# Kernel optimization log

Hardware: AMD Instinct MI355X
Metric: run time of the kernel (lower is better)

Reference implementation:

```python
import jax, jax.numpy as jnp
from jax import lax
import numpy as np

B, T, C = 8, 16384, 64
NUM_FILTERS, FILTER_SIZE = 64, 5
LEAKY_SLOPE = 0.3  # keras activation 'leaky_relu' default negative_slope


def setup_inputs() -> dict:
    key = jax.random.key(0)
    k1, k2, k3 = jax.random.split(key, 3)
    x = jax.random.normal(k1, (B, T, C), dtype=jnp.float32)
    interp_weights = jax.random.normal(k2, (C,), dtype=jnp.float32)
    # Conv1D kernel layout: [filter_size, in_channels, out_channels]
    conv_kernel = jax.random.normal(k3, (FILTER_SIZE, C, NUM_FILTERS), dtype=jnp.float32) * 0.05
    conv_bias = jnp.zeros((NUM_FILTERS,), dtype=jnp.float32)
    return {"x": x, "interp_weights": interp_weights,
            "conv_kernel": conv_kernel, "conv_bias": conv_bias}


def reference(x, interp_weights, conv_kernel, conv_bias):
    # Sigmoid gate per channel
    w = jax.nn.sigmoid(interp_weights)  # [C]
    # The diag conv2d (filter [1,2,C,C], SAME) is: blend[t] = w*x[t] + (1-w)*x[t+1]
    # (TF SAME for even width pads one zero frame on the right)
    x_next = jnp.concatenate([x[:, 1:, :], jnp.zeros_like(x[:, :1, :])], axis=1)
    blend = w * x + (1.0 - w) * x_next  # [B, T, C]
    # Interleave: even positions original, odd positions blended -> [B, 2T, C]
    up = jnp.stack([x, blend], axis=2).reshape(B, 2 * T, C)
    # Conv1D(num_filters, filter_size, padding='same', stride 1) + leaky_relu
    y = lax.conv_general_dilated(
        up, conv_kernel,
        window_strides=(1,), padding='SAME',
        dimension_numbers=('NWC', 'WIO', 'NWC'))
    y = y + conv_bias
    return jnp.where(y >= 0, y, LEAKY_SLOPE * y)
```

## Files before the change

### kernel.cpp

```cpp
#include <hip/hip_runtime.h>
#include <hip/hip_bf16.h>
#include <cstdint>


#define T_ 16384
#define TWO_T 32768
#define WSLICE 1376
#define XSTRIDE 72

typedef __bf16 bf16x8 __attribute__((ext_vector_type(8)));
typedef float  f32x4  __attribute__((ext_vector_type(4)));
typedef unsigned short u16x8 __attribute__((ext_vector_type(8)));
typedef unsigned short u16x4 __attribute__((ext_vector_type(4)));

__device__ __forceinline__ unsigned short f2bf(float f) {
    union { float f; uint32_t u; } v; v.f = f;
    uint32_t u = v.u;
    return (unsigned short)((u + 0x7FFFu + ((u >> 16) & 1u)) >> 16);
}

__device__ __forceinline__ float sigmoidf_(float z) {
    return 1.0f / (1.0f + expf(-z));
}

__global__ void lu_prep_kernel(const float* __restrict__ iw,
                               const float* __restrict__ ck,
                               const float* __restrict__ x,
                               unsigned short* __restrict__ bp,
                               float* __restrict__ corrf) {
    int fi = blockIdx.x;
    int l  = threadIdx.x;
    if (fi < 56) {
        int phase, ks, nt;
        if (fi < 24) { phase = 0; ks = fi >> 2; nt = fi & 3; }
        else         { phase = 1; ks = (fi - 24) >> 2; nt = (fi - 24) & 3; }
        int tap = ks >> 1;
        int n   = nt * 16 + (l & 15);
        int c0  = ((ks & 1) << 5) + ((l >> 4) << 3);
        u16x8 pk;
#pragma unroll
        for (int i = 0; i < 8; ++i) {
            int c = c0 + i;
            float w = sigmoidf_(iw[c]);
            float v;
            #define CK(k) ck[((k) * 64 + c) * 64 + n]
            if (phase == 0) {
                if (tap == 0)      v = CK(0) + w * CK(1);
                else if (tap == 1) v = (1.f - w) * CK(1) + CK(2) + w * CK(3);
                else               v = (1.f - w) * CK(3) + CK(4);
            } else {
                if (tap == 0)      v = w * CK(0);
                else if (tap == 1) v = (1.f - w) * CK(0) + CK(1) + w * CK(2);
                else if (tap == 2) v = (1.f - w) * CK(2) + CK(3) + w * CK(4);
                else               v = (1.f - w) * CK(4);
            }
            #undef CK
            pk[i] = f2bf(v);
        }
        *(u16x8*)(bp + (((size_t)fi * 64) + l) * 8) = pk;
    } else {
        int b = fi - 56;
        int f = l;
        float cE = 0.f, cO = 0.f;
        for (int c = 0; c < 64; ++c) {
            float w = sigmoidf_(iw[c]);
            float g = (1.f - w) * x[(size_t)b * T_ * 64 + c];
            cE += ck[(64 + c) * 64 + f] * g;
            cO += ck[c * 64 + f] * g;
        }
        corrf[b * 128 + f]      = cE;
        corrf[b * 128 + 64 + f] = cO;
    }
}

__global__ __launch_bounds__(256) void lu_main_kernel(
        const float* __restrict__ x,
        const unsigned short* __restrict__ bp,
        const float* __restrict__ corrf,
        const float* __restrict__ bias,
        float* __restrict__ out) {
    __shared__ __align__(16) unsigned short xl[4][WSLICE];

    const int wid  = blockIdx.x;
    const int b    = wid >> 10;
    const int win  = wid & 1023;
    const int tw0  = win << 4;
    const int tid  = threadIdx.x;
    const int lane = tid & 63;
    const int wv   = tid >> 6;

    unsigned short* xw = &xl[wv][0];

#pragma unroll
    for (int it = 0; it < 5; ++it) {
        int idx = it * 64 + lane;
        if (idx < 304) {
            int j  = idx >> 4;
            int c4 = (idx & 15) << 2;
            int gf = tw0 - 1 + j;
            float4 v = make_float4(0.f, 0.f, 0.f, 0.f);
            if (gf >= 0 && gf < T_)
                v = *(const float4*)(x + ((size_t)b * T_ + gf) * 64 + c4);
            u16x4 pk;
            pk[0] = f2bf(v.x); pk[1] = f2bf(v.y);
            pk[2] = f2bf(v.z); pk[3] = f2bf(v.w);
            *(u16x4*)(xw + j * XSTRIDE + c4) = pk;
        }
    }

    bf16x8 Be[6], Bo[8];
#pragma unroll
    for (int ks = 0; ks < 6; ++ks)
        Be[ks] = __builtin_bit_cast(bf16x8,
            *(const u16x8*)(bp + (((size_t)(ks * 4 + wv)) * 64 + lane) * 8));
#pragma unroll
    for (int ks = 0; ks < 8; ++ks)
        Bo[ks] = __builtin_bit_cast(bf16x8,
            *(const u16x8*)(bp + (((size_t)(24 + ks * 4 + wv)) * 64 + lane) * 8));

    const int   f      = (wv << 4) + (lane & 15);
    const float bias_f = bias[f];
    const int   arow   = lane & 15;
    const int   ac0    = (lane >> 4) << 3;

    bf16x8 Af[4][2];
#pragma unroll
    for (int tap = 0; tap < 4; ++tap)
#pragma unroll
        for (int h = 0; h < 2; ++h)
            Af[tap][h] = __builtin_bit_cast(bf16x8,
                *(const u16x8*)(xw + (arow + tap) * XSTRIDE + (h << 5) + ac0));

    f32x4 accE = {0.f, 0.f, 0.f, 0.f};
#pragma unroll
    for (int ks = 0; ks < 6; ++ks)
        accE = __builtin_amdgcn_mfma_f32_16x16x32_bf16(
                Af[ks >> 1][ks & 1], Be[ks], accE, 0, 0, 0);
    f32x4 accO = {0.f, 0.f, 0.f, 0.f};
#pragma unroll
    for (int ks = 0; ks < 8; ++ks)
        accO = __builtin_amdgcn_mfma_f32_16x16x32_bf16(
                Af[ks >> 1][ks & 1], Bo[ks], accO, 0, 0, 0);

    if (win == 0) {
        float cE = corrf[b * 128 + f];
        float cO = corrf[b * 128 + 64 + f];
        if ((lane >> 4) == 0) {
            accE[0] -= cE;
            accO[0] -= cO;
        }
    }

    const size_t ob = ((size_t)b * TWO_T + ((size_t)tw0 << 1)) * 64 + f;
#pragma unroll
    for (int i = 0; i < 4; ++i) {
        int r2 = (((lane >> 4) << 2) + i) << 1;
        float vE = accE[i] + bias_f;
        vE = vE >= 0.f ? vE : 0.3f * vE;
        out[ob + (size_t)r2 * 64] = vE;
        float vO = accO[i] + bias_f;
        vO = vO >= 0.f ? vO : 0.3f * vO;
        out[ob + (size_t)(r2 + 1) * 64] = vO;
    }
}

extern "C" void kernel_launch(void* const* d_in, const int* in_sizes, int n_in,
                              void* d_out, int out_size, void* d_ws, size_t ws_size,
                              hipStream_t stream) {
    (void)in_sizes; (void)n_in; (void)out_size; (void)ws_size;
    const float* x    = (const float*)d_in[0];
    const float* iw   = (const float*)d_in[1];
    const float* ck   = (const float*)d_in[2];
    const float* bias = (const float*)d_in[3];
    float* out = (float*)d_out;
    unsigned short* bp = (unsigned short*)d_ws;
    float* corrf = (float*)((char*)d_ws + 57344);

    lu_prep_kernel<<<64, 64, 0, stream>>>(iw, ck, x, bp, corrf);
    lu_main_kernel<<<8192, 256, 0, stream>>>(x, bp, corrf, bias, out);
}
```

Before: 39.84 us.

## Process four time windows per block with register-prefetched loads of the next window

Each block now handles 64 time steps as four 16-step windows instead of one, so the B-fragment weight loads are amortized over four windows. Global loads for the next window are issued into registers before the MFMAs of the current window run, to overlap memory latency with compute. The grid shrinks from 8192 to 2048 blocks, launch bounds add an occupancy hint, and the bf16 conversion uses the native cast. Risks include more register pressure and fewer blocks for latency hiding. There is also no barrier between a wave's LDS reads and its next overwrite of the same slice, which relies on in-order execution within a wave.

```diff
diff --git a/kernel.cpp b/kernel.cpp
--- a/kernel.cpp
+++ b/kernel.cpp
@@ -5,22 +5,22 @@
 
 #define T_ 16384
 #define TWO_T 32768
-#define WSLICE 1376
 #define XSTRIDE 72
+#define WSL 1376
 
 typedef __bf16 bf16x8 __attribute__((ext_vector_type(8)));
+typedef __bf16 bf16x4 __attribute__((ext_vector_type(4)));
 typedef float  f32x4  __attribute__((ext_vector_type(4)));
 typedef unsigned short u16x8 __attribute__((ext_vector_type(8)));
-typedef unsigned short u16x4 __attribute__((ext_vector_type(4)));
+
+__device__ __forceinline__ float sigmoidf_(float z) {
+    return 1.0f / (1.0f + expf(-z));
+}
 
 __device__ __forceinline__ unsigned short f2bf(float f) {
     union { float f; uint32_t u; } v; v.f = f;
     uint32_t u = v.u;
     return (unsigned short)((u + 0x7FFFu + ((u >> 16) & 1u)) >> 16);
-}
-
-__device__ __forceinline__ float sigmoidf_(float z) {
-    return 1.0f / (1.0f + expf(-z));
 }
 
 __global__ void lu_prep_kernel(const float* __restrict__ iw,
@@ -62,6 +62,7 @@
         int b = fi - 56;
         int f = l;
         float cE = 0.f, cO = 0.f;
+#pragma unroll
         for (int c = 0; c < 64; ++c) {
             float w = sigmoidf_(iw[c]);
             float g = (1.f - w) * x[(size_t)b * T_ * 64 + c];
@@ -73,40 +74,40 @@
     }
 }
 
-__global__ __launch_bounds__(256) void lu_main_kernel(
+__device__ __forceinline__ void issue_loads(const float* __restrict__ x,
+                                            int b, int t0, int lane, float4* ld) {
+#pragma unroll
+    for (int it = 0; it < 5; ++it) {
+        int idx = it * 64 + lane;
+        int j   = idx >> 4;
+        int c4  = (idx & 15) << 2;
+        int gf  = t0 - 1 + j;
+        float4 v = make_float4(0.f, 0.f, 0.f, 0.f);
+        if (idx < 304 && gf >= 0 && gf < T_)
+            v = *(const float4*)(x + ((size_t)b * T_ + gf) * 64 + c4);
+        ld[it] = v;
+    }
+}
+
+__global__ __launch_bounds__(256, 4) void lu_main_kernel(
         const float* __restrict__ x,
         const unsigned short* __restrict__ bp,
         const float* __restrict__ corrf,
         const float* __restrict__ bias,
         float* __restrict__ out) {
-    __shared__ __align__(16) unsigned short xl[4][WSLICE];
+    __shared__ __align__(16) unsigned short xl[4][WSL];
 
-    const int wid  = blockIdx.x;
-    const int b    = wid >> 10;
-    const int win  = wid & 1023;
-    const int tw0  = win << 4;
+    const int bid  = blockIdx.x;
+    const int b    = bid >> 8;
+    const int p0   = (bid & 255) << 6;
     const int tid  = threadIdx.x;
     const int lane = tid & 63;
     const int wv   = tid >> 6;
 
     unsigned short* xw = &xl[wv][0];
 
-#pragma unroll
-    for (int it = 0; it < 5; ++it) {
-        int idx = it * 64 + lane;
-        if (idx < 304) {
-            int j  = idx >> 4;
-            int c4 = (idx & 15) << 2;
-            int gf = tw0 - 1 + j;
-            float4 v = make_float4(0.f, 0.f, 0.f, 0.f);
-            if (gf >= 0 && gf < T_)
-                v = *(const float4*)(x + ((size_t)b * T_ + gf) * 64 + c4);
-            u16x4 pk;
-            pk[0] = f2bf(v.x); pk[1] = f2bf(v.y);
-            pk[2] = f2bf(v.z); pk[3] = f2bf(v.w);
-            *(u16x4*)(xw + j * XSTRIDE + c4) = pk;
-        }
-    }
+    float4 ld[5];
+    issue_loads(x, b, p0, lane, ld);
 
     bf16x8 Be[6], Bo[8];
 #pragma unroll
@@ -121,46 +122,57 @@
     const int   f      = (wv << 4) + (lane & 15);
     const float bias_f = bias[f];
     const int   arow   = lane & 15;
-    const int   ac0    = (lane >> 4) << 3;
+    const int   hi     = lane >> 4;
+    const int   ac0    = hi << 3;
 
-    bf16x8 Af[4][2];
+    for (int w = 0; w < 4; ++w) {
+        const int t0 = p0 + (w << 4);
+
 #pragma unroll
-    for (int tap = 0; tap < 4; ++tap)
+        for (int it = 0; it < 5; ++it) {
+            int idx = it * 64 + lane;
+            if (idx < 304) {
+                int j  = idx >> 4;
+                int c4 = (idx & 15) << 2;
+                bf16x4 pk;
+                pk[0] = (__bf16)ld[it].x; pk[1] = (__bf16)ld[it].y;
+                pk[2] = (__bf16)ld[it].z; pk[3] = (__bf16)ld[it].w;
+                *(bf16x4*)(xw + j * XSTRIDE + c4) = pk;
+            }
+        }
+
+        if (w < 3) issue_loads(x, b, p0 + ((w + 1) << 4), lane, ld);
+
+        f32x4 accE = {0.f, 0.f, 0.f, 0.f};
+        f32x4 accO = {0.f, 0.f, 0.f, 0.f};
 #pragma unroll
-        for (int h = 0; h < 2; ++h)
-            Af[tap][h] = __builtin_bit_cast(bf16x8,
-                *(const u16x8*)(xw + (arow + tap) * XSTRIDE + (h << 5) + ac0));
+        for (int tap = 0; tap < 4; ++tap)
+#pragma unroll
+            for (int h = 0; h < 2; ++h) {
+                bf16x8 a = __builtin_bit_cast(bf16x8,
+                    *(const u16x8*)(xw + (arow + tap) * XSTRIDE + (h << 5) + ac0));
+                int ks = tap * 2 + h;
+                if (tap < 3)
+                    accE = __builtin_amdgcn_mfma_f32_16x16x32_bf16(a, Be[ks], accE, 0, 0, 0);
+                accO = __builtin_amdgcn_mfma_f32_16x16x32_bf16(a, Bo[ks], accO, 0, 0, 0);
+            }
 
-    f32x4 accE = {0.f, 0.f, 0.f, 0.f};
+        if (((bid & 255) | w) == 0 && hi == 0) {
+            accE[0] -= corrf[b * 128 + f];
+            accO[0] -= corrf[b * 128 + 64 + f];
+        }
+
+        const size_t ob = ((size_t)b * TWO_T + ((size_t)t0 << 1)) * 64 + f;
 #pragma unroll
-    for (int ks = 0; ks < 6; ++ks)
-        accE = __builtin_amdgcn_mfma_f32_16x16x32_bf16(
-                Af[ks >> 1][ks & 1], Be[ks], accE, 0, 0, 0);
-    f32x4 accO = {0.f, 0.f, 0.f, 0.f};
-#pragma unroll
-    for (int ks = 0; ks < 8; ++ks)
-        accO = __builtin_amdgcn_mfma_f32_16x16x32_bf16(
-                Af[ks >> 1][ks & 1], Bo[ks], accO, 0, 0, 0);
-
-    if (win == 0) {
-        float cE = corrf[b * 128 + f];
-        float cO = corrf[b * 128 + 64 + f];
-        if ((lane >> 4) == 0) {
-            accE[0] -= cE;
-            accO[0] -= cO;
+        for (int i = 0; i < 4; ++i) {
+            int r2 = ((hi << 2) + i) << 1;
+            float vE = accE[i] + bias_f;
+            vE = vE >= 0.f ? vE : 0.3f * vE;
+            out[ob + (size_t)r2 * 64] = vE;
+            float vO = accO[i] + bias_f;
+            vO = vO >= 0.f ? vO : 0.3f * vO;
+            out[ob + (size_t)(r2 + 1) * 64] = vO;
         }
-    }
-
-    const size_t ob = ((size_t)b * TWO_T + ((size_t)tw0 << 1)) * 64 + f;
-#pragma unroll
-    for (int i = 0; i < 4; ++i) {
-        int r2 = (((lane >> 4) << 2) + i) << 1;
-        float vE = accE[i] + bias_f;
-        vE = vE >= 0.f ? vE : 0.3f * vE;
-        out[ob + (size_t)r2 * 64] = vE;
-        float vO = accO[i] + bias_f;
-        vO = vO >= 0.f ? vO : 0.3f * vO;
-        out[ob + (size_t)(r2 + 1) * 64] = vO;
     }
 }
 
@@ -177,5 +189,5 @@
     float* corrf = (float*)((char*)d_ws + 57344);
 
     lu_prep_kernel<<<64, 64, 0, stream>>>(iw, ck, x, bp, corrf);
-    lu_main_kernel<<<8192, 256, 0, stream>>>(x, bp, corrf, bias, out);
+    lu_main_kernel<<<2048, 256, 0, stream>>>(x, bp, corrf, bias, out);
 }
```

Result: faster. 32.33 us (-18.9%).
